# Kernel tuning notes

Hardware: AMD Instinct MI355X
Metric: run time of the kernel (lower is better)

Reference implementation:

```python
import jax, jax.numpy as jnp
import numpy as np

B, N, K, E, H, V = 128, 256, 4, 300, 150, 32000  # batch, nodes/tree, max children, embed, hidden, vocab
DELTA = 1.0


def setup_inputs() -> dict:
    key = jax.random.key(0)
    ks = jax.random.split(key, 8)
    query = jax.random.randint(ks[0], (B, N), 0, V, dtype=jnp.int32)
    pos = jax.random.randint(ks[1], (B, N), 0, V, dtype=jnp.int32)
    neg = jax.random.randint(ks[2], (B, N), 0, V, dtype=jnp.int32)
    # Complete K-ary tree over N nodes: children of node t are {K*t+1, ..., K*t+K} < N; root = node 0.
    ch = np.full((N, K), -1, dtype=np.int32)
    for t in range(N):
        for j in range(K):
            c = K * t + 1 + j
            if c < N:
                ch[t, j] = c
    children = jnp.asarray(ch)
    emb = jax.random.normal(ks[3], (V, E), dtype=jnp.float32) * 0.02
    W_iou = jax.random.normal(ks[4], (E, 3 * H), dtype=jnp.float32) * 0.05
    U_iou = jax.random.normal(ks[5], (H, 3 * H), dtype=jnp.float32) * 0.05
    b_iou = jnp.zeros((3 * H,), jnp.float32)
    W_f = jax.random.normal(ks[6], (E, H), dtype=jnp.float32) * 0.05
    U_f = jax.random.normal(ks[7], (H, H), dtype=jnp.float32) * 0.05
    b_f = jnp.zeros((H,), jnp.float32)
    return {"query": query, "pos": pos, "neg": neg, "children": children,
            "emb": emb, "W_iou": W_iou, "U_iou": U_iou, "b_iou": b_iou,
            "W_f": W_f, "U_f": U_f, "b_f": b_f}


def _childsum_treelstm(x, children, W_iou, U_iou, b_iou, W_f, U_f, b_f):
    """x: [B, N, E] node embeddings. Returns root (c, h): each [B, H]."""
    Bn, Nn, _ = x.shape
    Hh = U_f.shape[0]
    h0 = jnp.zeros((Bn, Nn, Hh), x.dtype)
    c0 = jnp.zeros((Bn, Nn, Hh), x.dtype)

    def step(carry, t):
        h_all, c_all = carry
        ch = children[t]                        # [K] child indices, -1 = padding
        mask = (ch >= 0)
        idx = jnp.where(mask, ch, 0)
        m = mask.astype(x.dtype)[None, :, None]  # [1, K, 1]
        h_k = h_all[:, idx] * m                 # [B, K, H]
        c_k = c_all[:, idx] * m
        h_sum = h_k.sum(axis=1)                 # child-sum h_tilde [B, H]
        x_t = x[:, t]                           # [B, E]
        iou = x_t @ W_iou + h_sum @ U_iou + b_iou
        i, o, u = jnp.split(iou, 3, axis=-1)
        i = jax.nn.sigmoid(i)
        o = jax.nn.sigmoid(o)
        u = jnp.tanh(u)
        # per-child forget gates: f_jk = sigmoid(W_f x_j + U_f h_k + b_f)
        f = jax.nn.sigmoid((x_t @ W_f + b_f)[:, None, :] + h_k @ U_f)  # [B, K, H]
        c_t = i * u + (f * c_k).sum(axis=1)     # c_k already masked
        h_t = o * jnp.tanh(c_t)
        return (h_all.at[:, t].set(h_t), c_all.at[:, t].set(c_t)), None

    # children have larger indices than parents -> process N-1 .. 0 (root last)
    (h_all, c_all), _ = jax.lax.scan(step, (h0, c0), jnp.arange(Nn - 1, -1, -1))
    return c_all[:, 0], h_all[:, 0]


def _cosine(a, b):
    num = (a * b).sum(-1)
    den = jnp.sqrt((a * a).sum(-1) * (b * b).sum(-1)) + 1e-8
    return num / den


def reference(query, pos, neg, children, emb, W_iou, U_iou, b_iou, W_f, U_f, b_f):
    qc, _ = _childsum_treelstm(emb[query], children, W_iou, U_iou, b_iou, W_f, U_f, b_f)
    pc, _ = _childsum_treelstm(emb[pos], children, W_iou, U_iou, b_iou, W_f, U_f, b_f)
    nc, _ = _childsum_treelstm(emb[neg], children, W_iou, U_iou, b_iou, W_f, U_f, b_f)
    a = _cosine(qc, pc)  # [B]
    b = _cosine(qc, nc)  # [B]
    return jax.nn.relu(DELTA - a + b)
```

## Files before the change

### kernel.cpp

```cpp
#include <hip/hip_runtime.h>
#include <hip/hip_bf16.h>

typedef short short8 __attribute__((ext_vector_type(8)));
typedef float floatx4 __attribute__((ext_vector_type(4)));
typedef unsigned short ushort;

#define Bb 128
#define Nn 256
#define Hh 150
#define HK 160
#define Vv 32000
#define NROW 384
#define PROJC 600
#define NINT 64
#define ZROW (Vv + NROW * NINT)

__device__ __forceinline__ float sigf(float x) { return 1.0f / (1.0f + __expf(-x)); }
__device__ __forceinline__ float tanhf_(float x) { return 1.0f - 2.0f / (__expf(2.0f * x) + 1.0f); }
__device__ __forceinline__ float bf2f(ushort s) { union { float f; unsigned u; } v; v.u = ((unsigned)s) << 16; return v.f; }
__device__ __forceinline__ ushort f2bf(float f) { __hip_bfloat16 h = __float2bfloat16(f); return *(ushort*)&h; }

__global__ __launch_bounds__(256) void k_prep(
    const float* __restrict__ W_iou, const float* __restrict__ W_f,
    const float* __restrict__ U_iou, const float* __restrict__ U_f,
    const float* __restrict__ b_iou, const float* __restrict__ b_f,
    short* __restrict__ Wt, short* __restrict__ Uti, short* __restrict__ Utf,
    float* __restrict__ biasw, ushort* __restrict__ h_u, float* __restrict__ c_u)
{
    int idx = blockIdx.x * 256 + threadIdx.x;
    const int nWt = 608 * 320, nUi = 464 * 160, nUf = 160 * 160;
    if (idx < nWt) {
        int n = idx / 320, k = idx % 320;
        float v = 0.f;
        if (k < 300) { if (n < 450) v = W_iou[k * 450 + n]; else if (n < 600) v = W_f[k * 150 + (n - 450)]; }
        Wt[idx] = (short)f2bf(v);
    } else if (idx < nWt + nUi) {
        int i2 = idx - nWt; int n = i2 / 160, k = i2 % 160;
        float v = (k < 150 && n < 450) ? U_iou[k * 450 + n] : 0.f;
        Uti[i2] = (short)f2bf(v);
    } else if (idx < nWt + nUi + nUf) {
        int i2 = idx - nWt - nUi; int n = i2 / 160, k = i2 % 160;
        float v = (k < 150) ? U_f[k * 150 + n] : 0.f;
        Utf[i2] = (short)f2bf(v);
    } else if (idx < nWt + nUi + nUf + 608) {
        int n = idx - nWt - nUi - nUf;
        biasw[n] = n < 450 ? b_iou[n] : (n < 600 ? b_f[n - 450] : 0.f);
    } else if (idx < nWt + nUi + nUf + 608 + HK) {
        int k = idx - (nWt + nUi + nUf + 608);
        h_u[(long)ZROW * HK + k] = 0;
        c_u[(long)ZROW * HK + k] = 0.f;
    }
}

__global__ __launch_bounds__(256) void k_vproj(
    const float* __restrict__ emb, const short* __restrict__ Wt,
    const float* __restrict__ biasw, ushort* __restrict__ proj)
{
    __shared__ __align__(16) short As[32 * 328];
    const int tid = threadIdx.x;
    const int v0 = blockIdx.x * 32;

    for (int i = tid; i < 32 * 80; i += 256) {
        int r = i / 80, q = i % 80, k0 = q * 4;
        short4 sv;
        if (k0 < 300) {
            float4 x = *(const float4*)(emb + (long)(v0 + r) * 300 + k0);
            sv.x = (short)f2bf(x.x); sv.y = (short)f2bf(x.y);
            sv.z = (short)f2bf(x.z); sv.w = (short)f2bf(x.w);
        } else sv = make_short4(0, 0, 0, 0);
        *(short4*)&As[r * 328 + k0] = sv;
    }
    __syncthreads();

    const int w = tid >> 6, lane = tid & 63;
    const int m = lane & 15, kq = (lane >> 4) * 8;

    short8 a0[10], a1[10];
    #pragma unroll
    for (int ks = 0; ks < 10; ks++) {
        a0[ks] = *(const short8*)&As[m * 328 + kq + ks * 32];
        a1[ks] = *(const short8*)&As[(16 + m) * 328 + kq + ks * 32];
    }

    for (int nt = w; nt < 38; nt += 4) {
        int col = nt * 16 + m;
        const short* bp = Wt + (long)col * 320 + kq;
        floatx4 acc0 = {0.f, 0.f, 0.f, 0.f}, acc1 = {0.f, 0.f, 0.f, 0.f};
        #pragma unroll
        for (int ks = 0; ks < 10; ks++) {
            short8 b = *(const short8*)(bp + ks * 32);
            acc0 = __builtin_amdgcn_mfma_f32_16x16x32_bf16(a0[ks], b, acc0, 0, 0, 0);
            acc1 = __builtin_amdgcn_mfma_f32_16x16x32_bf16(a1[ks], b, acc1, 0, 0, 0);
        }
        if (col < PROJC) {
            float bias = biasw[col];
            int rb = (lane >> 4) * 4;
            #pragma unroll
            for (int reg = 0; reg < 4; reg++) {
                proj[(long)(v0 + rb + reg) * PROJC + col]      = f2bf(acc0[reg] + bias);
                proj[(long)(v0 + 16 + rb + reg) * PROJC + col] = f2bf(acc1[reg] + bias);
            }
        }
    }
}

__global__ __launch_bounds__(256) void k_vleaf(
    const ushort* __restrict__ proj, ushort* __restrict__ h_u, float* __restrict__ c_u)
{
    int idx = blockIdx.x * 256 + threadIdx.x;
    int v = idx / 20, k0 = (idx % 20) * 8;
    const ushort* pr = proj + (long)v * PROJC;
    ushort hv[8]; float cvv[8];
    #pragma unroll
    for (int e = 0; e < 8; e++) {
        int k = k0 + e;
        if (k < Hh) {
            float iv = sigf(bf2f(pr[k]));
            float ov = sigf(bf2f(pr[150 + k]));
            float uv = tanhf_(bf2f(pr[300 + k]));
            float cc = iv * uv;
            cvv[e] = cc;
            hv[e] = f2bf(ov * tanhf_(cc));
        } else { cvv[e] = 0.f; hv[e] = 0; }
    }
    *(int4*)(h_u + (long)v * HK + k0) = *(int4*)hv;
    *(float4*)(c_u + (long)v * HK + k0)     = make_float4(cvv[0], cvv[1], cvv[2], cvv[3]);
    *(float4*)(c_u + (long)v * HK + k0 + 4) = make_float4(cvv[4], cvv[5], cvv[6], cvv[7]);
}

__global__ __launch_bounds__(256) void k_level(
    int t0,
    const int* __restrict__ tq, const int* __restrict__ tp, const int* __restrict__ tn,
    const int* __restrict__ children, const ushort* __restrict__ proj,
    const short* __restrict__ Uti, const short* __restrict__ Utf,
    ushort* __restrict__ h_u, float* __restrict__ c_u)
{
    __shared__ __align__(16) short As[5][16][168];
    __shared__ int idx_s[16][4];
    __shared__ int tok_s[16];

    const int tid = threadIdx.x;
    const int t = t0 + blockIdx.x / 24;
    const int r0 = (blockIdx.x % 24) * 16;

    if (tid < 64) {
        int r = tid >> 2, j = tid & 3;
        int rg = r0 + r, g = rg >> 7, b = rg & 127;
        const int* tok = (g == 0) ? tq : (g == 1 ? tp : tn);
        int ch = children[t * 4 + j];
        int idx;
        if (ch < 0)        idx = ZROW;
        else if (ch >= 64) idx = tok[b * Nn + ch];
        else               idx = Vv + rg * NINT + ch;
        idx_s[r][j] = idx;
        if (j == 0) tok_s[r] = tok[b * Nn + t];
    }
    __syncthreads();

    for (int i = tid; i < 16 * 20; i += 256) {
        int r = i / 20, k0 = (i % 20) * 8;
        int4 v0 = *(const int4*)(h_u + (long)idx_s[r][0] * HK + k0);
        int4 v1 = *(const int4*)(h_u + (long)idx_s[r][1] * HK + k0);
        int4 v2 = *(const int4*)(h_u + (long)idx_s[r][2] * HK + k0);
        int4 v3 = *(const int4*)(h_u + (long)idx_s[r][3] * HK + k0);
        *(int4*)&As[1][r][k0] = v0;
        *(int4*)&As[2][r][k0] = v1;
        *(int4*)&As[3][r][k0] = v2;
        *(int4*)&As[4][r][k0] = v3;
        ushort s[8];
        const ushort* p0 = (const ushort*)&v0; const ushort* p1 = (const ushort*)&v1;
        const ushort* p2 = (const ushort*)&v2; const ushort* p3 = (const ushort*)&v3;
        #pragma unroll
        for (int e = 0; e < 8; e++)
            s[e] = f2bf(bf2f(p0[e]) + bf2f(p1[e]) + bf2f(p2[e]) + bf2f(p3[e]));
        *(int4*)&As[0][r][k0] = *(int4*)s;
    }
    __syncthreads();

    const int w = tid >> 6, lane = tid & 63;
    const int m = lane & 15, kq = (lane >> 4) * 8;

    for (int nt = w; nt < 10; nt += 4) {
        int col = nt * 16 + m;
        const short* bi  = Uti + (long)(col) * HK + kq;
        const short* bo  = Uti + (long)(150 + col) * HK + kq;
        const short* bu  = Uti + (long)(300 + col) * HK + kq;
        const short* bff = Utf + (long)col * HK + kq;
        floatx4 ai = {0.f,0.f,0.f,0.f}, ao = ai, au = ai;
        floatx4 af0 = ai, af1 = ai, af2 = ai, af3 = ai;
        #pragma unroll
        for (int ks = 0; ks < 5; ks++) {
            short8 asum = *(const short8*)&As[0][m][kq + ks * 32];
            short8 ac0  = *(const short8*)&As[1][m][kq + ks * 32];
            short8 ac1  = *(const short8*)&As[2][m][kq + ks * 32];
            short8 ac2  = *(const short8*)&As[3][m][kq + ks * 32];
            short8 ac3  = *(const short8*)&As[4][m][kq + ks * 32];
            short8 vbi = *(const short8*)(bi + ks * 32);
            short8 vbo = *(const short8*)(bo + ks * 32);
            short8 vbu = *(const short8*)(bu + ks * 32);
            short8 vbf = *(const short8*)(bff + ks * 32);
            ai  = __builtin_amdgcn_mfma_f32_16x16x32_bf16(asum, vbi, ai, 0, 0, 0);
            ao  = __builtin_amdgcn_mfma_f32_16x16x32_bf16(asum, vbo, ao, 0, 0, 0);
            au  = __builtin_amdgcn_mfma_f32_16x16x32_bf16(asum, vbu, au, 0, 0, 0);
            af0 = __builtin_amdgcn_mfma_f32_16x16x32_bf16(ac0,  vbf, af0, 0, 0, 0);
            af1 = __builtin_amdgcn_mfma_f32_16x16x32_bf16(ac1,  vbf, af1, 0, 0, 0);
            af2 = __builtin_amdgcn_mfma_f32_16x16x32_bf16(ac2,  vbf, af2, 0, 0, 0);
            af3 = __builtin_amdgcn_mfma_f32_16x16x32_bf16(ac3,  vbf, af3, 0, 0, 0);
        }

        int rbase = (lane >> 4) * 4;
        if (col < Hh) {
            #pragma unroll
            for (int reg = 0; reg < 4; reg++) {
                int r = rbase + reg, rg = r0 + r;
                const ushort* pr = proj + (long)tok_s[r] * PROJC;
                float iv = sigf(bf2f(pr[col])        + ai[reg]);
                float ov = sigf(bf2f(pr[150 + col])  + ao[reg]);
                float uv = tanhf_(bf2f(pr[300 + col]) + au[reg]);
                float fpre = bf2f(pr[450 + col]);
                float cv = iv * uv;
                cv = fmaf(sigf(fpre + af0[reg]), c_u[(long)idx_s[r][0] * HK + col], cv);
                cv = fmaf(sigf(fpre + af1[reg]), c_u[(long)idx_s[r][1] * HK + col], cv);
                cv = fmaf(sigf(fpre + af2[reg]), c_u[(long)idx_s[r][2] * HK + col], cv);
                cv = fmaf(sigf(fpre + af3[reg]), c_u[(long)idx_s[r][3] * HK + col], cv);
                long o = (long)(Vv + rg * NINT + t) * HK + col;
                c_u[o] = cv;
                h_u[o] = f2bf(ov * tanhf_(cv));
            }
        } else {
            #pragma unroll
            for (int reg = 0; reg < 4; reg++) {
                long o = (long)(Vv + (r0 + rbase + reg) * NINT + t) * HK + col;
                c_u[o] = 0.f; h_u[o] = 0;
            }
        }
    }
}

__global__ __launch_bounds__(64) void k_cos(const float* __restrict__ c_u, float* __restrict__ out)
{
    int b = blockIdx.x, tid = threadIdx.x;
    const float* qc = c_u + (long)(Vv + (0 * Bb + b) * NINT) * HK;
    const float* pc = c_u + (long)(Vv + (1 * Bb + b) * NINT) * HK;
    const float* nc = c_u + (long)(Vv + (2 * Bb + b) * NINT) * HK;
    float qp = 0, qn = 0, qq = 0, pp = 0, nn2 = 0;
    for (int k = tid; k < Hh; k += 64) {
        float qv = qc[k], pv = pc[k], nv = nc[k];
        qp += qv * pv; qn += qv * nv; qq += qv * qv; pp += pv * pv; nn2 += nv * nv;
    }
    #pragma unroll
    for (int off = 32; off > 0; off >>= 1) {
        qp += __shfl_down(qp, off, 64);
        qn += __shfl_down(qn, off, 64);
        qq += __shfl_down(qq, off, 64);
        pp += __shfl_down(pp, off, 64);
        nn2 += __shfl_down(nn2, off, 64);
    }
    if (tid == 0) {
        float a = qp / (sqrtf(qq * pp) + 1e-8f);
        float d = qn / (sqrtf(qq * nn2) + 1e-8f);
        out[b] = fmaxf(0.0f, 1.0f - a + d);
    }
}

extern "C" void kernel_launch(void* const* d_in, const int* in_sizes, int n_in,
                              void* d_out, int out_size, void* d_ws, size_t ws_size,
                              hipStream_t stream)
{
    const int*   tq       = (const int*)d_in[0];
    const int*   tp       = (const int*)d_in[1];
    const int*   tn       = (const int*)d_in[2];
    const int*   children = (const int*)d_in[3];
    const float* emb      = (const float*)d_in[4];
    const float* W_iou    = (const float*)d_in[5];
    const float* U_iou    = (const float*)d_in[6];
    const float* b_iou    = (const float*)d_in[7];
    const float* W_f      = (const float*)d_in[8];
    const float* U_f      = (const float*)d_in[9];
    const float* b_f      = (const float*)d_in[10];
    float* out = (float*)d_out;

    char* ws = (char*)d_ws;
    ushort* proj  = (ushort*)ws;
    ushort* h_u   = (ushort*)(ws + 38400000);
    float*  c_u   = (float*)(ws + 56504640);
    short*  Wt    = (short*)(ws + 92713920);
    short*  Uti   = (short*)(ws + 93103040);
    short*  Utf   = (short*)(ws + 93251520);
    float*  biasw = (float*)(ws + 93302720);

    k_prep<<<1153, 256, 0, stream>>>(W_iou, W_f, U_iou, U_f, b_iou, b_f,
                                     Wt, Uti, Utf, biasw, h_u, c_u);
    k_vproj<<<Vv / 32, 256, 0, stream>>>(emb, Wt, biasw, proj);
    k_vleaf<<<2500, 256, 0, stream>>>(proj, h_u, c_u);
    k_level<<<43 * 24, 256, 0, stream>>>(21, tq, tp, tn, children, proj, Uti, Utf, h_u, c_u);
    k_level<<<16 * 24, 256, 0, stream>>>(5,  tq, tp, tn, children, proj, Uti, Utf, h_u, c_u);
    k_level<<<4 * 24, 256, 0, stream>>>(1,   tq, tp, tn, children, proj, Uti, Utf, h_u, c_u);
    k_level<<<1 * 24, 256, 0, stream>>>(0,   tq, tp, tn, children, proj, Uti, Utf, h_u, c_u);
    k_cos<<<Bb, 64, 0, stream>>>(c_u, out);
}
```

Before: 272.8 us.

## Fuse leaf cell computation into vocab projection with gate-aligned padded layout

Pads the projection layout so each gate (i, o, u, f) sits in its own 160-column segment. Each wave can then compute all four gates for one hidden column and apply the leaf LSTM cell inline, which removes the separate k_vleaf kernel and its re-read of proj. The level kernel now prefetches the proj and child c values into registers before the MFMA loop, so their latency overlaps the matmul. The cost is a wider proj buffer (640 columns instead of 600), more accumulator registers in k_vproj, and transcendental work added to the projection epilogue.

```diff
diff --git a/kernel.cpp b/kernel.cpp
--- a/kernel.cpp
+++ b/kernel.cpp
@@ -11,7 +11,7 @@
 #define HK 160
 #define Vv 32000
 #define NROW 384
-#define PROJC 600
+#define PROJC 640
 #define NINT 64
 #define ZROW (Vv + NROW * NINT)
 
@@ -28,11 +28,17 @@
     float* __restrict__ biasw, ushort* __restrict__ h_u, float* __restrict__ c_u)
 {
     int idx = blockIdx.x * 256 + threadIdx.x;
-    const int nWt = 608 * 320, nUi = 464 * 160, nUf = 160 * 160;
+    const int nWt = PROJC * 320, nUi = 464 * 160, nUf = 160 * 160;
     if (idx < nWt) {
         int n = idx / 320, k = idx % 320;
+        int seg = n / 160, cc = n % 160;
         float v = 0.f;
-        if (k < 300) { if (n < 450) v = W_iou[k * 450 + n]; else if (n < 600) v = W_f[k * 150 + (n - 450)]; }
+        if (k < 300 && cc < 150) {
+            if (seg == 0)      v = W_iou[k * 450 + cc];
+            else if (seg == 1) v = W_iou[k * 450 + 150 + cc];
+            else if (seg == 2) v = W_iou[k * 450 + 300 + cc];
+            else               v = W_f[k * 150 + cc];
+        }
         Wt[idx] = (short)f2bf(v);
     } else if (idx < nWt + nUi) {
         int i2 = idx - nWt; int n = i2 / 160, k = i2 % 160;
@@ -42,11 +48,12 @@
         int i2 = idx - nWt - nUi; int n = i2 / 160, k = i2 % 160;
         float v = (k < 150) ? U_f[k * 150 + n] : 0.f;
         Utf[i2] = (short)f2bf(v);
-    } else if (idx < nWt + nUi + nUf + 608) {
+    } else if (idx < nWt + nUi + nUf + PROJC) {
         int n = idx - nWt - nUi - nUf;
-        biasw[n] = n < 450 ? b_iou[n] : (n < 600 ? b_f[n - 450] : 0.f);
-    } else if (idx < nWt + nUi + nUf + 608 + HK) {
-        int k = idx - (nWt + nUi + nUf + 608);
+        int seg = n / 160, cc = n % 160;
+        biasw[n] = (cc < 150) ? (seg < 3 ? b_iou[seg * 150 + cc] : b_f[cc]) : 0.f;
+    } else if (idx < nWt + nUi + nUf + PROJC + HK) {
+        int k = idx - (nWt + nUi + nUf + PROJC);
         h_u[(long)ZROW * HK + k] = 0;
         c_u[(long)ZROW * HK + k] = 0.f;
     }
@@ -54,7 +61,8 @@
 
 __global__ __launch_bounds__(256) void k_vproj(
     const float* __restrict__ emb, const short* __restrict__ Wt,
-    const float* __restrict__ biasw, ushort* __restrict__ proj)
+    const float* __restrict__ biasw, ushort* __restrict__ proj,
+    ushort* __restrict__ h_u, float* __restrict__ c_u)
 {
     __shared__ __align__(16) short As[32 * 328];
     const int tid = threadIdx.x;
@@ -82,50 +90,52 @@
         a1[ks] = *(const short8*)&As[(16 + m) * 328 + kq + ks * 32];
     }
 
-    for (int nt = w; nt < 38; nt += 4) {
-        int col = nt * 16 + m;
+    for (int j = w; j < 10; j += 4) {
+        int col = j * 16 + m;
         const short* bp = Wt + (long)col * 320 + kq;
-        floatx4 acc0 = {0.f, 0.f, 0.f, 0.f}, acc1 = {0.f, 0.f, 0.f, 0.f};
+        floatx4 acc[4][2];
+        #pragma unroll
+        for (int s = 0; s < 4; s++) { acc[s][0] = {0.f,0.f,0.f,0.f}; acc[s][1] = {0.f,0.f,0.f,0.f}; }
         #pragma unroll
         for (int ks = 0; ks < 10; ks++) {
-            short8 b = *(const short8*)(bp + ks * 32);
-            acc0 = __builtin_amdgcn_mfma_f32_16x16x32_bf16(a0[ks], b, acc0, 0, 0, 0);
-            acc1 = __builtin_amdgcn_mfma_f32_16x16x32_bf16(a1[ks], b, acc1, 0, 0, 0);
-        }
-        if (col < PROJC) {
-            float bias = biasw[col];
-            int rb = (lane >> 4) * 4;
+            short8 b0 = *(const short8*)(bp + 0 * 160 * 320 + ks * 32);
+            short8 b1 = *(const short8*)(bp + 1 * 160 * 320 + ks * 32);
+            short8 b2 = *(const short8*)(bp + 2 * 160 * 320 + ks * 32);
+            short8 b3 = *(const short8*)(bp + 3 * 160 * 320 + ks * 32);
+            acc[0][0] = __builtin_amdgcn_mfma_f32_16x16x32_bf16(a0[ks], b0, acc[0][0], 0, 0, 0);
+            acc[0][1] = __builtin_amdgcn_mfma_f32_16x16x32_bf16(a1[ks], b0, acc[0][1], 0, 0, 0);
+            acc[1][0] = __builtin_amdgcn_mfma_f32_16x16x32_bf16(a0[ks], b1, acc[1][0], 0, 0, 0);
+            acc[1][1] = __builtin_amdgcn_mfma_f32_16x16x32_bf16(a1[ks], b1, acc[1][1], 0, 0, 0);
+            acc[2][0] = __builtin_amdgcn_mfma_f32_16x16x32_bf16(a0[ks], b2, acc[2][0], 0, 0, 0);
+            acc[2][1] = __builtin_amdgcn_mfma_f32_16x16x32_bf16(a1[ks], b2, acc[2][1], 0, 0, 0);
+            acc[3][0] = __builtin_amdgcn_mfma_f32_16x16x32_bf16(a0[ks], b3, acc[3][0], 0, 0, 0);
+            acc[3][1] = __builtin_amdgcn_mfma_f32_16x16x32_bf16(a1[ks], b3, acc[3][1], 0, 0, 0);
+        }
+
+        float bi_ = biasw[col], bo_ = biasw[160 + col];
+        float bu_ = biasw[320 + col], bf_ = biasw[480 + col];
+        int rb = (lane >> 4) * 4;
+        #pragma unroll
+        for (int g = 0; g < 2; g++) {
             #pragma unroll
             for (int reg = 0; reg < 4; reg++) {
-                proj[(long)(v0 + rb + reg) * PROJC + col]      = f2bf(acc0[reg] + bias);
-                proj[(long)(v0 + 16 + rb + reg) * PROJC + col] = f2bf(acc1[reg] + bias);
+                long row = v0 + g * 16 + rb + reg;
+                float pi = acc[0][g][reg] + bi_;
+                float po = acc[1][g][reg] + bo_;
+                float pu = acc[2][g][reg] + bu_;
+                float pf = acc[3][g][reg] + bf_;
+                ushort* pr = proj + row * PROJC;
+                pr[col]       = f2bf(pi);
+                pr[160 + col] = f2bf(po);
+                pr[320 + col] = f2bf(pu);
+                pr[480 + col] = f2bf(pf);
+                float iv = sigf(pi), ov = sigf(po), uv = tanhf_(pu);
+                float cc = iv * uv;
+                c_u[row * HK + col] = cc;
+                h_u[row * HK + col] = f2bf(ov * tanhf_(cc));
             }
         }
     }
-}
-
-__global__ __launch_bounds__(256) void k_vleaf(
-    const ushort* __restrict__ proj, ushort* __restrict__ h_u, float* __restrict__ c_u)
-{
-    int idx = blockIdx.x * 256 + threadIdx.x;
-    int v = idx / 20, k0 = (idx % 20) * 8;
-    const ushort* pr = proj + (long)v * PROJC;
-    ushort hv[8]; float cvv[8];
-    #pragma unroll
-    for (int e = 0; e < 8; e++) {
-        int k = k0 + e;
-        if (k < Hh) {
-            float iv = sigf(bf2f(pr[k]));
-            float ov = sigf(bf2f(pr[150 + k]));
-            float uv = tanhf_(bf2f(pr[300 + k]));
-            float cc = iv * uv;
-            cvv[e] = cc;
-            hv[e] = f2bf(ov * tanhf_(cc));
-        } else { cvv[e] = 0.f; hv[e] = 0; }
-    }
-    *(int4*)(h_u + (long)v * HK + k0) = *(int4*)hv;
-    *(float4*)(c_u + (long)v * HK + k0)     = make_float4(cvv[0], cvv[1], cvv[2], cvv[3]);
-    *(float4*)(c_u + (long)v * HK + k0 + 4) = make_float4(cvv[4], cvv[5], cvv[6], cvv[7]);
 }
 
 __global__ __launch_bounds__(256) void k_level(
@@ -179,9 +189,24 @@
 
     const int w = tid >> 6, lane = tid & 63;
     const int m = lane & 15, kq = (lane >> 4) * 8;
+    const int rbase = (lane >> 4) * 4;
 
     for (int nt = w; nt < 10; nt += 4) {
         int col = nt * 16 + m;
+
+        ushort pg[4][4]; float cg[4][4];
+        #pragma unroll
+        for (int reg = 0; reg < 4; reg++) {
+            const ushort* pr = proj + (long)tok_s[rbase + reg] * PROJC;
+            pg[0][reg] = pr[col];
+            pg[1][reg] = pr[160 + col];
+            pg[2][reg] = pr[320 + col];
+            pg[3][reg] = pr[480 + col];
+            #pragma unroll
+            for (int j = 0; j < 4; j++)
+                cg[j][reg] = c_u[(long)idx_s[rbase + reg][j] * HK + col];
+        }
+
         const short* bi  = Uti + (long)(col) * HK + kq;
         const short* bo  = Uti + (long)(150 + col) * HK + kq;
         const short* bu  = Uti + (long)(300 + col) * HK + kq;
@@ -208,21 +233,19 @@
             af3 = __builtin_amdgcn_mfma_f32_16x16x32_bf16(ac3,  vbf, af3, 0, 0, 0);
         }
 
-        int rbase = (lane >> 4) * 4;
         if (col < Hh) {
             #pragma unroll
             for (int reg = 0; reg < 4; reg++) {
-                int r = rbase + reg, rg = r0 + r;
-                const ushort* pr = proj + (long)tok_s[r] * PROJC;
-                float iv = sigf(bf2f(pr[col])        + ai[reg]);
-                float ov = sigf(bf2f(pr[150 + col])  + ao[reg]);
-                float uv = tanhf_(bf2f(pr[300 + col]) + au[reg]);
-                float fpre = bf2f(pr[450 + col]);
+                int rg = r0 + rbase + reg;
+                float iv = sigf(bf2f(pg[0][reg])   + ai[reg]);
+                float ov = sigf(bf2f(pg[1][reg])   + ao[reg]);
+                float uv = tanhf_(bf2f(pg[2][reg]) + au[reg]);
+                float fpre = bf2f(pg[3][reg]);
                 float cv = iv * uv;
-                cv = fmaf(sigf(fpre + af0[reg]), c_u[(long)idx_s[r][0] * HK + col], cv);
-                cv = fmaf(sigf(fpre + af1[reg]), c_u[(long)idx_s[r][1] * HK + col], cv);
-                cv = fmaf(sigf(fpre + af2[reg]), c_u[(long)idx_s[r][2] * HK + col], cv);
-                cv = fmaf(sigf(fpre + af3[reg]), c_u[(long)idx_s[r][3] * HK + col], cv);
+                cv = fmaf(sigf(fpre + af0[reg]), cg[0][reg], cv);
+                cv = fmaf(sigf(fpre + af1[reg]), cg[1][reg], cv);
+                cv = fmaf(sigf(fpre + af2[reg]), cg[2][reg], cv);
+                cv = fmaf(sigf(fpre + af3[reg]), cg[3][reg], cv);
                 long o = (long)(Vv + rg * NINT + t) * HK + col;
                 c_u[o] = cv;
                 h_u[o] = f2bf(ov * tanhf_(cv));
@@ -282,17 +305,16 @@
 
     char* ws = (char*)d_ws;
     ushort* proj  = (ushort*)ws;
-    ushort* h_u   = (ushort*)(ws + 38400000);
-    float*  c_u   = (float*)(ws + 56504640);
-    short*  Wt    = (short*)(ws + 92713920);
-    short*  Uti   = (short*)(ws + 93103040);
-    short*  Utf   = (short*)(ws + 93251520);
-    float*  biasw = (float*)(ws + 93302720);
-
-    k_prep<<<1153, 256, 0, stream>>>(W_iou, W_f, U_iou, U_f, b_iou, b_f,
+    ushort* h_u   = (ushort*)(ws + 40960000);
+    float*  c_u   = (float*)(ws + 59064640);
+    short*  Wt    = (short*)(ws + 95273920);
+    short*  Uti   = (short*)(ws + 95683520);
+    short*  Utf   = (short*)(ws + 95832000);
+    float*  biasw = (float*)(ws + 95883200);
+
+    k_prep<<<1194, 256, 0, stream>>>(W_iou, W_f, U_iou, U_f, b_iou, b_f,
                                      Wt, Uti, Utf, biasw, h_u, c_u);
-    k_vproj<<<Vv / 32, 256, 0, stream>>>(emb, Wt, biasw, proj);
-    k_vleaf<<<2500, 256, 0, stream>>>(proj, h_u, c_u);
+    k_vproj<<<Vv / 32, 256, 0, stream>>>(emb, Wt, biasw, proj, h_u, c_u);
     k_level<<<43 * 24, 256, 0, stream>>>(21, tq, tp, tn, children, proj, Uti, Utf, h_u, c_u);
     k_level<<<16 * 24, 256, 0, stream>>>(5,  tq, tp, tn, children, proj, Uti, Utf, h_u, c_u);
     k_level<<<4 * 24, 256, 0, stream>>>(1,   tq, tp, tn, children, proj, Uti, Utf, h_u, c_u);
```

Result: slower. 286.6 us (+5.1%).
